# Performance work log

Measured on AMD Instinct MI355X. Metric: run time of the kernel, lower is better.

## Reference

```python
import jax, jax.numpy as jnp
import numpy as np

V, E, H, L = 32000, 256, 512, 1
B, S, T = 64, 64, 20


def setup_inputs() -> dict:
    key = jax.random.key(0)
    ks = jax.random.split(key, 12)
    return {
        "tgt_batch": jax.random.randint(ks[0], (B, T), 0, V),
        "len_src_batch": jax.random.randint(ks[1], (B,), 1, S + 1).astype(jnp.int32),
        "len_tgt_batch": jnp.full((B,), T, dtype=jnp.int32),
        "enc_final": jax.random.normal(ks[2], (L, B, H), jnp.float32),
        "enc_outputs": jax.random.normal(ks[3], (S, B, H), jnp.float32),
        "teacher_forcing": 1,
        "emb": jax.random.normal(ks[4], (V, E), jnp.float32) * 0.05,
        "W_ih": jax.random.normal(ks[5], (3 * H, E + H), jnp.float32) * 0.03,
        "W_hh": jax.random.normal(ks[6], (3 * H, H), jnp.float32) * 0.03,
        "b_ih": jnp.zeros((3 * H,), jnp.float32),
        "b_hh": jnp.zeros((3 * H,), jnp.float32),
        "W_attn": jax.random.normal(ks[7], (H, H), jnp.float32) * 0.03,
        "W_concat": jax.random.normal(ks[8], (H, 2 * H), jnp.float32) * 0.03,
        "b_concat": jnp.zeros((H,), jnp.float32),
        "W_out": jax.random.normal(ks[9], (V, H), jnp.float32) * 0.03,
        "b_out": jnp.zeros((V,), jnp.float32),
    }


def reference(tgt_batch, len_src_batch, len_tgt_batch, enc_final, enc_outputs,
              teacher_forcing, emb, W_ih, W_hh, b_ih, b_hh, W_attn,
              W_concat, b_concat, W_out, b_out):
    # source-length mask (B,S)
    src_mask = jnp.arange(S)[None, :] < len_src_batch[:, None]
    enc_bsh = enc_outputs.transpose(1, 0, 2)              # (B,S,H)
    enc_proj = jnp.einsum('bsh,gh->bsg', enc_bsh, W_attn)  # general attn: precompute W_a @ enc
    tgt_tb = tgt_batch.T                                   # (T,B)

    def gru_cell(x, h):
        gi = x @ W_ih.T + b_ih
        gh = h @ W_hh.T + b_hh
        ir, iz, inn = jnp.split(gi, 3, axis=-1)
        hr, hz, hn = jnp.split(gh, 3, axis=-1)
        r = jax.nn.sigmoid(ir + hr)
        z = jax.nn.sigmoid(iz + hz)
        n = jnp.tanh(inn + r * hn)
        return (1.0 - z) * n + z * h

    def step(carry, tok):
        h, attn_h = carry
        x = jnp.concatenate([emb[tok], attn_h], axis=-1)   # (B,E+H)
        h = gru_cell(x, h)                                 # (B,H)
        score = jnp.einsum('bh,bsh->bs', h, enc_proj)      # (B,S)
        score = jnp.where(src_mask, score, -1e9)
        aw = jax.nn.softmax(score, axis=-1)                # align weights
        ctx = jnp.einsum('bs,bsh->bh', aw, enc_bsh)        # bmm context
        attn_h = jnp.tanh(jnp.concatenate([h, ctx], -1) @ W_concat.T + b_concat)
        logits = attn_h @ W_out.T + b_out                  # (B,V)
        logp = jax.nn.log_softmax(logits, axis=-1)
        word = jnp.argmax(logp, axis=-1)
        return (h, attn_h), (logp, word)

    h0 = enc_final[0]                                      # L=1, D=1 -> (B,H)
    attn0 = jnp.zeros((B, H), jnp.float32)
    # teacher_forcing == 1: input at step t is gold token tgt[t], t = 0..T-2
    _, (dec_outputs, dec_words) = jax.lax.scan(step, (h0, attn0), tgt_tb[:-1])
    return dec_outputs, dec_words
```

## Files before the change

kernel.cpp:

```cpp
#include <hip/hip_runtime.h>
#include <math.h>

#define TSTEPS 19
#define NB 64
#define NS 64
#define NT 20
#define NH 512
#define NE 256
#define NV 32000

__device__ __forceinline__ float ldg_sys(const float* p) {
  return __hip_atomic_load(p, __ATOMIC_RELAXED, __HIP_MEMORY_SCOPE_SYSTEM);
}
__device__ __forceinline__ void stg_sys(float* p, float v) {
  __hip_atomic_store(p, v, __ATOMIC_RELAXED, __HIP_MEMORY_SCOPE_SYSTEM);
}
__device__ __forceinline__ int ldi_sys(const int* p) {
  return __hip_atomic_load(p, __ATOMIC_RELAXED, __HIP_MEMORY_SCOPE_SYSTEM);
}
__device__ __forceinline__ void sti_sys(int* p, int v) {
  __hip_atomic_store(p, v, __ATOMIC_RELAXED, __HIP_MEMORY_SCOPE_SYSTEM);
}
__device__ __forceinline__ void vmfence() {
  asm volatile("s_waitcnt vmcnt(0)" ::: "memory");
}
__device__ __forceinline__ void flag_publish(int* f) {
  vmfence();
  __syncthreads();
  if (threadIdx.x == 0) sti_sys(f, 1);
  asm volatile("" ::: "memory");
}
__device__ __forceinline__ void wait_n(const int* f, int n) {
  if (threadIdx.x < 64) {
    for (;;) {
      int ok = 1;
      for (int i = threadIdx.x; i < n; i += 64) ok &= ldi_sys(f + i);
      if (__all(ok)) break;
      __builtin_amdgcn_s_sleep(1);
    }
  }
  __syncthreads();
  asm volatile("" ::: "memory");
}

__global__ __launch_bounds__(256) void linear_kernel(
    const float* __restrict__ A, int lda,
    const float* __restrict__ W, int ldw,
    const float* __restrict__ bias,
    float* __restrict__ C, int ldc,
    int K, int act)
{
  __shared__ float As[16][68];
  __shared__ float Ws[16][132];
  const int tid = threadIdx.x;
  const int m0 = blockIdx.y * 64;
  const int n0 = blockIdx.x * 128;
  const int lr = tid >> 2;
  const int lc = (tid & 3) << 2;
  const int tm = tid & 15;
  const int tn = tid >> 4;

  float acc[4][8];
#pragma unroll
  for (int i = 0; i < 4; ++i)
#pragma unroll
    for (int j = 0; j < 8; ++j) acc[i][j] = 0.f;

  const float* Ar  = A + (size_t)(m0 + lr) * lda + lc;
  const float* Wr0 = W + (size_t)(n0 + lr) * ldw + lc;
  const float* Wr1 = W + (size_t)(n0 + 64 + lr) * ldw + lc;

  for (int kk = 0; kk < K; kk += 16) {
    float4 av = *(const float4*)(Ar + kk);
    float4 w0 = *(const float4*)(Wr0 + kk);
    float4 w1 = *(const float4*)(Wr1 + kk);
    As[lc+0][lr] = av.x; As[lc+1][lr] = av.y; As[lc+2][lr] = av.z; As[lc+3][lr] = av.w;
    Ws[lc+0][lr] = w0.x; Ws[lc+1][lr] = w0.y; Ws[lc+2][lr] = w0.z; Ws[lc+3][lr] = w0.w;
    Ws[lc+0][64+lr] = w1.x; Ws[lc+1][64+lr] = w1.y; Ws[lc+2][64+lr] = w1.z; Ws[lc+3][64+lr] = w1.w;
    __syncthreads();
#pragma unroll
    for (int k = 0; k < 16; ++k) {
      float4 a4 = *(const float4*)&As[k][tm * 4];
      float4 b4 = *(const float4*)&Ws[k][tn * 8];
      float4 b5 = *(const float4*)&Ws[k][tn * 8 + 4];
      float a[4] = {a4.x, a4.y, a4.z, a4.w};
      float b[8] = {b4.x, b4.y, b4.z, b4.w, b5.x, b5.y, b5.z, b5.w};
#pragma unroll
      for (int i = 0; i < 4; ++i)
#pragma unroll
        for (int j = 0; j < 8; ++j)
          acc[i][j] = fmaf(a[i], b[j], acc[i][j]);
    }
    __syncthreads();
  }

#pragma unroll
  for (int i = 0; i < 4; ++i) {
    int m = m0 + tm * 4 + i;
    float* crow = C + (size_t)m * ldc + n0 + tn * 8;
    float vv[8];
#pragma unroll
    for (int j = 0; j < 8; ++j) {
      float v = acc[i][j];
      if (bias) v += bias[n0 + tn * 8 + j];
      if (act == 1) v = tanhf(v);
      vv[j] = v;
    }
    *(float4*)(crow)     = make_float4(vv[0], vv[1], vv[2], vv[3]);
    *(float4*)(crow + 4) = make_float4(vv[4], vv[5], vv[6], vv[7]);
  }
}

__global__ __launch_bounds__(256) void emb_linear_kernel(
    const float* __restrict__ emb, const int* __restrict__ tgt,
    const float* __restrict__ W_ih, const float* __restrict__ b_ih,
    float* __restrict__ C)
{
  __shared__ float As[16][68];
  __shared__ float Ws[16][132];
  const int tid = threadIdx.x;
  const int m0 = blockIdx.y * 64;
  const int n0 = blockIdx.x * 128;
  const int lr = tid >> 2;
  const int lc = (tid & 3) << 2;
  const int tm = tid & 15;
  const int tn = tid >> 4;

  float acc[4][8];
#pragma unroll
  for (int i = 0; i < 4; ++i)
#pragma unroll
    for (int j = 0; j < 8; ++j) acc[i][j] = 0.f;

  const int row = m0 + lr;
  const int tok = tgt[(row & 63) * NT + (row >> 6)];
  const float* Ar  = emb + (size_t)tok * NE + lc;
  const float* Wr0 = W_ih + (size_t)(n0 + lr) * 768 + lc;
  const float* Wr1 = W_ih + (size_t)(n0 + 64 + lr) * 768 + lc;

  for (int kk = 0; kk < NE; kk += 16) {
    float4 av = *(const float4*)(Ar + kk);
    float4 w0 = *(const float4*)(Wr0 + kk);
    float4 w1 = *(const float4*)(Wr1 + kk);
    As[lc+0][lr] = av.x; As[lc+1][lr] = av.y; As[lc+2][lr] = av.z; As[lc+3][lr] = av.w;
    Ws[lc+0][lr] = w0.x; Ws[lc+1][lr] = w0.y; Ws[lc+2][lr] = w0.z; Ws[lc+3][lr] = w0.w;
    Ws[lc+0][64+lr] = w1.x; Ws[lc+1][64+lr] = w1.y; Ws[lc+2][64+lr] = w1.z; Ws[lc+3][64+lr] = w1.w;
    __syncthreads();
#pragma unroll
    for (int k = 0; k < 16; ++k) {
      float4 a4 = *(const float4*)&As[k][tm * 4];
      float4 b4 = *(const float4*)&Ws[k][tn * 8];
      float4 b5 = *(const float4*)&Ws[k][tn * 8 + 4];
      float a[4] = {a4.x, a4.y, a4.z, a4.w};
      float b[8] = {b4.x, b4.y, b4.z, b4.w, b5.x, b5.y, b5.z, b5.w};
#pragma unroll
      for (int i = 0; i < 4; ++i)
#pragma unroll
        for (int j = 0; j < 8; ++j)
          acc[i][j] = fmaf(a[i], b[j], acc[i][j]);
    }
    __syncthreads();
  }

#pragma unroll
  for (int i = 0; i < 4; ++i) {
    int m = m0 + tm * 4 + i;
    float* crow = C + (size_t)m * 1536 + n0 + tn * 8;
    float vv[8];
#pragma unroll
    for (int j = 0; j < 8; ++j) vv[j] = acc[i][j] + b_ih[n0 + tn * 8 + j];
    *(float4*)(crow)     = make_float4(vv[0], vv[1], vv[2], vv[3]);
    *(float4*)(crow + 4) = make_float4(vv[4], vv[5], vv[6], vv[7]);
  }
}

__global__ __launch_bounds__(256) void logits_kernel(
    const float* __restrict__ A, const float* __restrict__ W,
    const float* __restrict__ bias, float* __restrict__ C)
{
  const int bfl = blockIdx.x;
  const int xcd = bfl & 7;
  const int jj = bfl >> 3;
  const int mt = jj % 19;
  const int nt = xcd * 32 + jj / 19;
  if (nt >= 250) return;
  const int m0 = mt * 64;
  const int n0 = nt * 128;

  __shared__ float As[16][68];
  __shared__ float Ws[16][132];
  const int tid = threadIdx.x;
  const int lr = tid >> 2;
  const int lc = (tid & 3) << 2;
  const int tm = tid & 15;
  const int tn = tid >> 4;

  float acc[4][8];
#pragma unroll
  for (int i = 0; i < 4; ++i)
#pragma unroll
    for (int j = 0; j < 8; ++j) acc[i][j] = 0.f;

  const float* Ar  = A + (size_t)(m0 + lr) * NH + lc;
  const float* Wr0 = W + (size_t)(n0 + lr) * NH + lc;
  const float* Wr1 = W + (size_t)(n0 + 64 + lr) * NH + lc;

  for (int kk = 0; kk < NH; kk += 16) {
    float4 av = *(const float4*)(Ar + kk);
    float4 w0 = *(const float4*)(Wr0 + kk);
    float4 w1 = *(const float4*)(Wr1 + kk);
    As[lc+0][lr] = av.x; As[lc+1][lr] = av.y; As[lc+2][lr] = av.z; As[lc+3][lr] = av.w;
    Ws[lc+0][lr] = w0.x; Ws[lc+1][lr] = w0.y; Ws[lc+2][lr] = w0.z; Ws[lc+3][lr] = w0.w;
    Ws[lc+0][64+lr] = w1.x; Ws[lc+1][64+lr] = w1.y; Ws[lc+2][64+lr] = w1.z; Ws[lc+3][64+lr] = w1.w;
    __syncthreads();
#pragma unroll
    for (int k = 0; k < 16; ++k) {
      float4 a4 = *(const float4*)&As[k][tm * 4];
      float4 b4 = *(const float4*)&Ws[k][tn * 8];
      float4 b5 = *(const float4*)&Ws[k][tn * 8 + 4];
      float a[4] = {a4.x, a4.y, a4.z, a4.w};
      float b[8] = {b4.x, b4.y, b4.z, b4.w, b5.x, b5.y, b5.z, b5.w};
#pragma unroll
      for (int i = 0; i < 4; ++i)
#pragma unroll
        for (int j = 0; j < 8; ++j)
          acc[i][j] = fmaf(a[i], b[j], acc[i][j]);
    }
    __syncthreads();
  }

#pragma unroll
  for (int i = 0; i < 4; ++i) {
    int m = m0 + tm * 4 + i;
    float* crow = C + (size_t)m * NV + n0 + tn * 8;
    float vv[8];
#pragma unroll
    for (int j = 0; j < 8; ++j) vv[j] = acc[i][j] + bias[n0 + tn * 8 + j];
    *(float4*)(crow)     = make_float4(vv[0], vv[1], vv[2], vv[3]);
    *(float4*)(crow + 4) = make_float4(vv[4], vv[5], vv[6], vv[7]);
  }
}

template <int SYSA>
__device__ __forceinline__ void gemm_tile2(
    const float* __restrict__ Asrc, const float* __restrict__ W, int ldw,
    float* __restrict__ Cdst, int n0, int k0,
    float (*As)[68], float (*Ws)[68])
{
  const int tid = threadIdx.x;
  const int l = tid & 63, w = tid >> 6;
  const int m = l, nq = w;
  const int wn = tid >> 4, wc = (tid & 15) << 2;
  const int q4 = (l & 15) << 2;
  float acc[4] = {0.f, 0.f, 0.f, 0.f};
  for (int kk = 0; kk < 256; kk += 64) {
    const int kb = k0 + kk;
#pragma unroll
    for (int i = 0; i < 4; ++i) {
      const int mi = 16 * w + 4 * i + (l >> 4);
      const float* src = Asrc + (size_t)mi * NH + kb + q4;
      float4 v;
      if (SYSA) {
        v.x = ldg_sys(src); v.y = ldg_sys(src + 1);
        v.z = ldg_sys(src + 2); v.w = ldg_sys(src + 3);
      } else {
        v = *(const float4*)src;
      }
      *(float4*)&As[mi][q4] = v;
    }
    *(float4*)&Ws[wn][wc] = *(const float4*)(W + (size_t)(n0 + wn) * ldw + kb + wc);
    __syncthreads();
#pragma unroll
    for (int q = 0; q < 16; ++q) {
      float4 a4 = *(const float4*)&As[m][q * 4];
#pragma unroll
      for (int j = 0; j < 4; ++j) {
        float4 w4 = *(const float4*)&Ws[nq * 4 + j][q * 4];
        acc[j] = fmaf(a4.x, w4.x, acc[j]);
        acc[j] = fmaf(a4.y, w4.y, acc[j]);
        acc[j] = fmaf(a4.z, w4.z, acc[j]);
        acc[j] = fmaf(a4.w, w4.w, acc[j]);
      }
    }
    __syncthreads();
  }
#pragma unroll
  for (int j = 0; j < 4; ++j)
    stg_sys(Cdst + (size_t)m * 1536 + n0 + nq * 4 + j, acc[j]);
}

__global__ __launch_bounds__(256) void recur_kernel(
    const float* __restrict__ gi_emb, float* __restrict__ giA2,
    float* __restrict__ ghA2, float* __restrict__ hglob,
    float* __restrict__ attn_arr, const float* __restrict__ enc_proj,
    const float* __restrict__ enc_proj2, const float* __restrict__ enc_final,
    const int* __restrict__ len_src, const float* __restrict__ W_ih,
    const float* __restrict__ W_hh, const float* __restrict__ b_hh,
    const float* __restrict__ W_concat, const float* __restrict__ b_concat,
    int* __restrict__ flags)
{
  const int blk = blockIdx.x;
  const int tid = threadIdx.x;
  __shared__ float As[64][68];
  __shared__ float Ws[16][68];
  __shared__ float hstate[NH];
  __shared__ float scs[NS];
  __shared__ float aw[NS];

  int* ghdone = flags;
  int* gidone = flags + 4096;
  int* hdone  = flags + 8192;
  int* adone  = flags + 10240;

  if (blk >= 64) {
    const int hj = blk - 64;
    const int n0 = (hj >> 1) * 16;
    const int kh = hj & 1;
    const int k0 = kh * 256;
    float* ghD = ghA2 + kh * 98304;
    float* giD = giA2 + kh * 98304;
    gemm_tile2<0>(enc_final, W_hh, NH, ghD, n0, k0, As, Ws);
    flag_publish(ghdone + hj);
    for (int t = 0; t + 1 < TSTEPS; ++t) {
      wait_n(hdone + t * 64, 64);
      gemm_tile2<1>(hglob, W_hh, NH, ghD, n0, k0, As, Ws);
      flag_publish(ghdone + (t + 1) * 192 + hj);
      wait_n(adone + t * 64, 64);
      gemm_tile2<1>(attn_arr + (size_t)t * NB * NH, W_ih + NE, NE + NH,
                    giD, n0, k0, As, Ws);
      flag_publish(gidone + (t + 1) * 192 + hj);
    }
    return;
  }

  const int b = blk;
  hstate[tid]       = enc_final[(size_t)b * NH + tid];
  hstate[tid + 256] = enc_final[(size_t)b * NH + tid + 256];
  __syncthreads();
  const int mylen = len_src[b];

  for (int t = 0; t < TSTEPS; ++t) {
    wait_n(ghdone + t * 192, 192);
    if (t > 0) wait_n(gidone + t * 192, 192);

    const float* ge = gi_emb + (size_t)(t * NB + b) * 1536;
#pragma unroll
    for (int hh = 0; hh < 2; ++hh) {
      const int j = tid + hh * 256;
      const size_t base = (size_t)b * 1536 + j;
      float gr = ge[j];
      float gz = ge[512 + j];
      float gn = ge[1024 + j];
      if (t > 0) {
        gr += ldg_sys(giA2 + base)        + ldg_sys(giA2 + 98304 + base);
        gz += ldg_sys(giA2 + base + 512)  + ldg_sys(giA2 + 98304 + base + 512);
        gn += ldg_sys(giA2 + base + 1024) + ldg_sys(giA2 + 98304 + base + 1024);
      }
      float hr = b_hh[j]        + ldg_sys(ghA2 + base)        + ldg_sys(ghA2 + 98304 + base);
      float hz = b_hh[512 + j]  + ldg_sys(ghA2 + base + 512)  + ldg_sys(ghA2 + 98304 + base + 512);
      float hn = b_hh[1024 + j] + ldg_sys(ghA2 + base + 1024) + ldg_sys(ghA2 + 98304 + base + 1024);
      float r = 1.f / (1.f + expf(-(gr + hr)));
      float z = 1.f / (1.f + expf(-(gz + hz)));
      float n = tanhf(gn + r * hn);
      float h = (1.f - z) * n + z * hstate[j];
      hstate[j] = h;
      stg_sys(hglob + (size_t)b * NH + j, h);
    }
    vmfence();
    __syncthreads();
    if (tid == 0) sti_sys(hdone + t * 64 + b, 1);

    {
      const int s = tid >> 2, sub = tid & 3;
      const float* ep = enc_proj + ((size_t)s * NB + b) * NH + sub * 4;
      float acc = 0.f;
#pragma unroll 8
      for (int i = 0; i < 32; ++i) {
        float4 e4 = *(const float4*)(ep + i * 16);
        float4 h4 = *(const float4*)&hstate[i * 16 + sub * 4];
        acc = fmaf(e4.x, h4.x, acc); acc = fmaf(e4.y, h4.y, acc);
        acc = fmaf(e4.z, h4.z, acc); acc = fmaf(e4.w, h4.w, acc);
      }
      acc += __shfl_xor(acc, 1);
      acc += __shfl_xor(acc, 2);
      if (sub == 0) scs[s] = acc;
    }
    __syncthreads();
    if (tid < 64) {
      float v = (tid < mylen) ? scs[tid] : -1e9f;
      float mm = v;
      for (int off = 32; off >= 1; off >>= 1) mm = fmaxf(mm, __shfl_xor(mm, off));
      float e = expf(v - mm);
      float ssum = e;
      for (int off = 32; off >= 1; off >>= 1) ssum += __shfl_xor(ssum, off);
      aw[tid] = e / ssum;
    }
    __syncthreads();
    float c0 = 0.f, c1 = 0.f;
#pragma unroll 4
    for (int s2 = 0; s2 < NS; ++s2) {
      const float w = aw[s2];
      const float* e2 = enc_proj2 + ((size_t)s2 * NB + b) * NH;
      c0 = fmaf(w, e2[tid], c0);
      c1 = fmaf(w, e2[tid + 256], c1);
    }
    float* at = attn_arr + ((size_t)t * NB + b) * NH;
#pragma unroll
    for (int h2 = 0; h2 < 2; ++h2) {
      const int n = tid + h2 * 256;
      const float* wr = W_concat + (size_t)n * (2 * NH);
      float acc = 0.f;
      for (int k = 0; k < NH; k += 4) {
        float4 w4 = *(const float4*)(wr + k);
        acc = fmaf(w4.x, hstate[k],     acc);
        acc = fmaf(w4.y, hstate[k + 1], acc);
        acc = fmaf(w4.z, hstate[k + 2], acc);
        acc = fmaf(w4.w, hstate[k + 3], acc);
      }
      acc += b_concat[n] + (h2 ? c1 : c0);
      stg_sys(at + n, tanhf(acc));
    }
    vmfence();
    __syncthreads();
    if (tid == 0) sti_sys(adone + t * 64 + b, 1);
  }
}

__global__ __launch_bounds__(256) void row_softmax_kernel(
    float* __restrict__ out, float* __restrict__ words)
{
  const int row = blockIdx.x;
  const int tid = threadIdx.x;
  float* p = out + (size_t)row * NV;
  __shared__ float sm[256];
  __shared__ int   si[256];
  __shared__ float ss[256];

  float mv = -INFINITY; int mi = 0; float s = 0.f;
  for (int i = tid; i < NV; i += 256) {
    float v = p[i];
    if (v > mv) {
      s = s * expf(mv - v) + 1.f;
      mv = v; mi = i;
    } else {
      s += expf(v - mv);
    }
  }
  sm[tid] = mv; si[tid] = mi; ss[tid] = s;
  __syncthreads();
  for (int off = 128; off >= 1; off >>= 1) {
    if (tid < off) {
      float m1 = sm[tid], m2 = sm[tid + off];
      float s1 = ss[tid], s2 = ss[tid + off];
      int   i1 = si[tid], i2 = si[tid + off];
      float M = fmaxf(m1, m2);
      ss[tid] = s1 * expf(m1 - M) + s2 * expf(m2 - M);
      if (m2 > m1 || (m2 == m1 && i2 < i1)) { sm[tid] = m2; si[tid] = i2; }
    }
    __syncthreads();
  }
  const float lse = sm[0] + logf(ss[0]);
  for (int i = tid; i < NV; i += 256) p[i] -= lse;
  if (tid == 0) words[row] = (float)si[0];
}

__global__ __launch_bounds__(256) void init_kernel(int* __restrict__ flags)
{
  int i = blockIdx.x * 256 + threadIdx.x;
  if (i < 12288)
    __hip_atomic_store(flags + i, 0, __ATOMIC_RELAXED, __HIP_MEMORY_SCOPE_SYSTEM);
}

extern "C" void kernel_launch(void* const* d_in, const int* in_sizes, int n_in,
                              void* d_out, int out_size, void* d_ws, size_t ws_size,
                              hipStream_t stream) {
  const int*   tgt       = (const int*)d_in[0];
  const int*   len_src   = (const int*)d_in[1];
  const float* enc_final = (const float*)d_in[3];
  const float* enc_out   = (const float*)d_in[4];
  const float* emb       = (const float*)d_in[6];
  const float* W_ih      = (const float*)d_in[7];
  const float* W_hh      = (const float*)d_in[8];
  const float* b_ih      = (const float*)d_in[9];
  const float* b_hh      = (const float*)d_in[10];
  const float* W_attn    = (const float*)d_in[11];
  const float* W_concat  = (const float*)d_in[12];
  const float* b_concat  = (const float*)d_in[13];
  const float* W_out     = (const float*)d_in[14];
  const float* b_out     = (const float*)d_in[15];
  float* out = (float*)d_out;

  float* ws = (float*)d_ws;
  float* enc_proj = ws;
  float* gi_emb   = ws + 2097152;
  float* attn_arr = ws + 3964928;

  const size_t LOGF = (size_t)TSTEPS * NB * NV;
  float* tail = out + (LOGF - 2560000);
  float* enc_proj2 = tail;
  float* giA2  = enc_proj2 + 2097152;
  float* ghA2  = giA2 + 196608;
  float* hglob = ghA2 + 196608;
  int*   flags = (int*)(hglob + 32768);

  init_kernel<<<48, 256, 0, stream>>>(flags);

  linear_kernel<<<dim3(4, 64), 256, 0, stream>>>(
      enc_out, 512, W_attn, 512, nullptr, enc_proj, 512, 512, 0);

  linear_kernel<<<dim3(4, 64), 256, 0, stream>>>(
      enc_out, 512, W_concat + 512, 1024, nullptr, enc_proj2, 512, 512, 0);

  emb_linear_kernel<<<dim3(12, 19), 256, 0, stream>>>(
      emb, tgt, W_ih, b_ih, gi_emb);

  void* kargs[] = {
    (void*)&gi_emb, (void*)&giA2, (void*)&ghA2, (void*)&hglob,
    (void*)&attn_arr, (void*)&enc_proj, (void*)&enc_proj2, (void*)&enc_final,
    (void*)&len_src, (void*)&W_ih, (void*)&W_hh, (void*)&b_hh,
    (void*)&W_concat, (void*)&b_concat, (void*)&flags
  };
  hipLaunchCooperativeKernel((const void*)recur_kernel, dim3(256), dim3(256),
                             kargs, 0, stream);

  logits_kernel<<<4864, 256, 0, stream>>>(attn_arr, W_out, b_out, out);

  row_softmax_kernel<<<TSTEPS * NB, 256, 0, stream>>>(
      out, out + LOGF);
}
```

Baseline: 2.252 ms.

## Split recurrent GEMM helpers into separate gh and gi block groups with vectorized coherent IO

Helper blocks inside the persistent cooperative recurrence kernel now split into two groups. One group (96 blocks) computes h@W_hh and a separate group computes attn@W_ih, so the two projections run concurrently instead of serially in the same blocks. Each helper tile now covers 32 columns and a 256-wide K slice loaded in one shot, removing the inner k-loop syncs. Scalar system-scope atomics are replaced with inline-asm dwordx4 loads and stores carrying sc0 sc1 bits, and the gate math is vectorized. This raises shared memory use per block (about 100KB) and relies on hand-written cache-coherence bits for correctness.

```diff
diff --git a/kernel.cpp b/kernel.cpp
--- a/kernel.cpp
+++ b/kernel.cpp
@@ -9,12 +9,8 @@
 #define NE 256
 #define NV 32000
 
-__device__ __forceinline__ float ldg_sys(const float* p) {
-  return __hip_atomic_load(p, __ATOMIC_RELAXED, __HIP_MEMORY_SCOPE_SYSTEM);
-}
-__device__ __forceinline__ void stg_sys(float* p, float v) {
-  __hip_atomic_store(p, v, __ATOMIC_RELAXED, __HIP_MEMORY_SCOPE_SYSTEM);
-}
+typedef float f32x4 __attribute__((ext_vector_type(4)));
+
 __device__ __forceinline__ int ldi_sys(const int* p) {
   return __hip_atomic_load(p, __ATOMIC_RELAXED, __HIP_MEMORY_SCOPE_SYSTEM);
 }
@@ -23,6 +19,9 @@
 }
 __device__ __forceinline__ void vmfence() {
   asm volatile("s_waitcnt vmcnt(0)" ::: "memory");
+}
+__device__ __forceinline__ void stg4(float* p, f32x4 v) {
+  asm volatile("global_store_dwordx4 %0, %1, off sc0 sc1" :: "v"(p), "v"(v) : "memory");
 }
 __device__ __forceinline__ void flag_publish(int* f) {
   vmfence();
@@ -242,51 +241,96 @@
 }
 
 template <int SYSA>
-__device__ __forceinline__ void gemm_tile2(
+__device__ __forceinline__ void gemm_helper(
     const float* __restrict__ Asrc, const float* __restrict__ W, int ldw,
     float* __restrict__ Cdst, int n0, int k0,
-    float (*As)[68], float (*Ws)[68])
+    float (*As)[260], float (*Ws)[260])
 {
   const int tid = threadIdx.x;
-  const int l = tid & 63, w = tid >> 6;
-  const int m = l, nq = w;
-  const int wn = tid >> 4, wc = (tid & 15) << 2;
-  const int q4 = (l & 15) << 2;
-  float acc[4] = {0.f, 0.f, 0.f, 0.f};
-  for (int kk = 0; kk < 256; kk += 64) {
-    const int kb = k0 + kk;
-#pragma unroll
-    for (int i = 0; i < 4; ++i) {
-      const int mi = 16 * w + 4 * i + (l >> 4);
-      const float* src = Asrc + (size_t)mi * NH + kb + q4;
-      float4 v;
-      if (SYSA) {
-        v.x = ldg_sys(src); v.y = ldg_sys(src + 1);
-        v.z = ldg_sys(src + 2); v.w = ldg_sys(src + 3);
-      } else {
-        v = *(const float4*)src;
-      }
-      *(float4*)&As[mi][q4] = v;
-    }
-    *(float4*)&Ws[wn][wc] = *(const float4*)(W + (size_t)(n0 + wn) * ldw + kb + wc);
-    __syncthreads();
-#pragma unroll
-    for (int q = 0; q < 16; ++q) {
-      float4 a4 = *(const float4*)&As[m][q * 4];
-#pragma unroll
-      for (int j = 0; j < 4; ++j) {
-        float4 w4 = *(const float4*)&Ws[nq * 4 + j][q * 4];
-        acc[j] = fmaf(a4.x, w4.x, acc[j]);
-        acc[j] = fmaf(a4.y, w4.y, acc[j]);
-        acc[j] = fmaf(a4.z, w4.z, acc[j]);
-        acc[j] = fmaf(a4.w, w4.w, acc[j]);
-      }
-    }
-    __syncthreads();
-  }
-#pragma unroll
-  for (int j = 0; j < 4; ++j)
-    stg_sys(Cdst + (size_t)m * 1536 + n0 + nq * 4 + j, acc[j]);
+  if (SYSA) {
+    const float* s[16];
+#pragma unroll
+    for (int i = 0; i < 16; ++i) {
+      const int f = tid + (i << 8);
+      s[i] = Asrc + (size_t)(f >> 6) * NH + k0 + ((f & 63) << 2);
+    }
+    f32x4 v0,v1,v2,v3,v4,v5,v6,v7,v8,v9,v10,v11,v12,v13,v14,v15;
+    asm volatile(
+      "global_load_dwordx4 %0, %8, off sc0 sc1\n\t"
+      "global_load_dwordx4 %1, %9, off sc0 sc1\n\t"
+      "global_load_dwordx4 %2, %10, off sc0 sc1\n\t"
+      "global_load_dwordx4 %3, %11, off sc0 sc1\n\t"
+      "global_load_dwordx4 %4, %12, off sc0 sc1\n\t"
+      "global_load_dwordx4 %5, %13, off sc0 sc1\n\t"
+      "global_load_dwordx4 %6, %14, off sc0 sc1\n\t"
+      "global_load_dwordx4 %7, %15, off sc0 sc1"
+      : "=&v"(v0),"=&v"(v1),"=&v"(v2),"=&v"(v3),
+        "=&v"(v4),"=&v"(v5),"=&v"(v6),"=&v"(v7)
+      : "v"(s[0]),"v"(s[1]),"v"(s[2]),"v"(s[3]),
+        "v"(s[4]),"v"(s[5]),"v"(s[6]),"v"(s[7])
+      : "memory");
+    asm volatile(
+      "global_load_dwordx4 %0, %8, off sc0 sc1\n\t"
+      "global_load_dwordx4 %1, %9, off sc0 sc1\n\t"
+      "global_load_dwordx4 %2, %10, off sc0 sc1\n\t"
+      "global_load_dwordx4 %3, %11, off sc0 sc1\n\t"
+      "global_load_dwordx4 %4, %12, off sc0 sc1\n\t"
+      "global_load_dwordx4 %5, %13, off sc0 sc1\n\t"
+      "global_load_dwordx4 %6, %14, off sc0 sc1\n\t"
+      "global_load_dwordx4 %7, %15, off sc0 sc1\n\t"
+      "s_waitcnt vmcnt(0)"
+      : "=&v"(v8),"=&v"(v9),"=&v"(v10),"=&v"(v11),
+        "=&v"(v12),"=&v"(v13),"=&v"(v14),"=&v"(v15)
+      : "v"(s[8]),"v"(s[9]),"v"(s[10]),"v"(s[11]),
+        "v"(s[12]),"v"(s[13]),"v"(s[14]),"v"(s[15])
+      : "memory");
+    __builtin_amdgcn_sched_barrier(0);
+    f32x4 vv[16] = {v0,v1,v2,v3,v4,v5,v6,v7,v8,v9,v10,v11,v12,v13,v14,v15};
+#pragma unroll
+    for (int i = 0; i < 16; ++i) {
+      const int f = tid + (i << 8);
+      *(f32x4*)&As[f >> 6][(f & 63) << 2] = vv[i];
+    }
+  } else {
+#pragma unroll
+    for (int i = 0; i < 16; ++i) {
+      const int f = tid + (i << 8);
+      *(f32x4*)&As[f >> 6][(f & 63) << 2] =
+          *(const f32x4*)(Asrc + (size_t)(f >> 6) * NH + k0 + ((f & 63) << 2));
+    }
+  }
+#pragma unroll
+  for (int i = 0; i < 8; ++i) {
+    const int f = tid + (i << 8);
+    *(f32x4*)&Ws[f >> 6][(f & 63) << 2] =
+        *(const f32x4*)(W + (size_t)(n0 + (f >> 6)) * ldw + k0 + ((f & 63) << 2));
+  }
+  __syncthreads();
+  const int tm = tid & 31, tn = tid >> 5;
+  float acc[2][4] = {{0.f,0.f,0.f,0.f},{0.f,0.f,0.f,0.f}};
+#pragma unroll 2
+  for (int q = 0; q < 64; ++q) {
+    f32x4 a0 = *(const f32x4*)&As[tm][q << 2];
+    f32x4 a1 = *(const f32x4*)&As[tm + 32][q << 2];
+#pragma unroll
+    for (int jj = 0; jj < 4; ++jj) {
+      f32x4 w4 = *(const f32x4*)&Ws[(tn << 2) + jj][q << 2];
+      float t0 = acc[0][jj];
+      t0 = fmaf(a0.x, w4.x, t0); t0 = fmaf(a0.y, w4.y, t0);
+      t0 = fmaf(a0.z, w4.z, t0); t0 = fmaf(a0.w, w4.w, t0);
+      acc[0][jj] = t0;
+      float t1 = acc[1][jj];
+      t1 = fmaf(a1.x, w4.x, t1); t1 = fmaf(a1.y, w4.y, t1);
+      t1 = fmaf(a1.z, w4.z, t1); t1 = fmaf(a1.w, w4.w, t1);
+      acc[1][jj] = t1;
+    }
+  }
+  __syncthreads();
+  f32x4 r0 = {acc[0][0], acc[0][1], acc[0][2], acc[0][3]};
+  f32x4 r1 = {acc[1][0], acc[1][1], acc[1][2], acc[1][3]};
+  float* p0 = Cdst + (size_t)tm * 1536 + n0 + (tn << 2);
+  stg4(p0, r0);
+  stg4(p0 + 32 * 1536, r1);
 }
 
 __global__ __launch_bounds__(256) void recur_kernel(
@@ -301,34 +345,35 @@
 {
   const int blk = blockIdx.x;
   const int tid = threadIdx.x;
-  __shared__ float As[64][68];
-  __shared__ float Ws[16][68];
+  __shared__ float As[64][260];
+  __shared__ float Ws[32][260];
   __shared__ float hstate[NH];
+  __shared__ float uext[NH];
   __shared__ float scs[NS];
   __shared__ float aw[NS];
 
-  int* ghdone = flags;
-  int* gidone = flags + 4096;
-  int* hdone  = flags + 8192;
-  int* adone  = flags + 10240;
-
+  if (blk >= 160) {
+    const int hj = blk - 160;
+    const int n0 = (hj >> 1) * 32, kh = hj & 1, k0 = kh * 256;
+    float* giD = giA2 + kh * 98304;
+    for (int t = 0; t + 1 < TSTEPS; ++t) {
+      wait_n(flags + 6400 + t * 64, 64);
+      gemm_helper<1>(attn_arr + (size_t)t * NB * NH, W_ih + NE, NE + NH,
+                     giD, n0, k0, As, Ws);
+      flag_publish(flags + (t + 1) * 256 + 96 + hj);
+    }
+    return;
+  }
   if (blk >= 64) {
     const int hj = blk - 64;
-    const int n0 = (hj >> 1) * 16;
-    const int kh = hj & 1;
-    const int k0 = kh * 256;
+    const int n0 = (hj >> 1) * 32, kh = hj & 1, k0 = kh * 256;
     float* ghD = ghA2 + kh * 98304;
-    float* giD = giA2 + kh * 98304;
-    gemm_tile2<0>(enc_final, W_hh, NH, ghD, n0, k0, As, Ws);
-    flag_publish(ghdone + hj);
+    gemm_helper<0>(enc_final, W_hh, NH, ghD, n0, k0, As, Ws);
+    flag_publish(flags + hj);
     for (int t = 0; t + 1 < TSTEPS; ++t) {
-      wait_n(hdone + t * 64, 64);
-      gemm_tile2<1>(hglob, W_hh, NH, ghD, n0, k0, As, Ws);
-      flag_publish(ghdone + (t + 1) * 192 + hj);
-      wait_n(adone + t * 64, 64);
-      gemm_tile2<1>(attn_arr + (size_t)t * NB * NH, W_ih + NE, NE + NH,
-                    giD, n0, k0, As, Ws);
-      flag_publish(gidone + (t + 1) * 192 + hj);
+      wait_n(flags + 5120 + t * 64, 64);
+      gemm_helper<1>(hglob, W_hh, NH, ghD, n0, k0, As, Ws);
+      flag_publish(flags + (t + 1) * 256 + hj);
     }
     return;
   }
@@ -340,35 +385,86 @@
   const int mylen = len_src[b];
 
   for (int t = 0; t < TSTEPS; ++t) {
-    wait_n(ghdone + t * 192, 192);
-    if (t > 0) wait_n(gidone + t * 192, 192);
-
-    const float* ge = gi_emb + (size_t)(t * NB + b) * 1536;
-#pragma unroll
-    for (int hh = 0; hh < 2; ++hh) {
-      const int j = tid + hh * 256;
+    if (t == 0) wait_n(flags, 96);
+    else        wait_n(flags + t * 256, 192);
+
+    if (tid < 128) {
+      const int j = tid << 2;
+      const float* ge = gi_emb + (size_t)(t * NB + b) * 1536;
+      f32x4 er = *(const f32x4*)(ge + j);
+      f32x4 ez = *(const f32x4*)(ge + 512 + j);
+      f32x4 en = *(const f32x4*)(ge + 1024 + j);
+      f32x4 br = *(const f32x4*)(b_hh + j);
+      f32x4 bz = *(const f32x4*)(b_hh + 512 + j);
+      f32x4 bn = *(const f32x4*)(b_hh + 1024 + j);
       const size_t base = (size_t)b * 1536 + j;
-      float gr = ge[j];
-      float gz = ge[512 + j];
-      float gn = ge[1024 + j];
+      f32x4 I0,I1,I2,I3,I4,I5, G0,G1,G2,G3,G4,G5;
       if (t > 0) {
-        gr += ldg_sys(giA2 + base)        + ldg_sys(giA2 + 98304 + base);
-        gz += ldg_sys(giA2 + base + 512)  + ldg_sys(giA2 + 98304 + base + 512);
-        gn += ldg_sys(giA2 + base + 1024) + ldg_sys(giA2 + 98304 + base + 1024);
+        const float* q0 = giA2 + base;          const float* q1 = q0 + 512;
+        const float* q2 = q0 + 1024;
+        const float* q3 = giA2 + 98304 + base;  const float* q4 = q3 + 512;
+        const float* q5 = q3 + 1024;
+        const float* r0 = ghA2 + base;          const float* r1 = r0 + 512;
+        const float* r2 = r0 + 1024;
+        const float* r3 = ghA2 + 98304 + base;  const float* r4 = r3 + 512;
+        const float* r5 = r3 + 1024;
+        asm volatile(
+          "global_load_dwordx4 %0, %12, off sc0 sc1\n\t"
+          "global_load_dwordx4 %1, %13, off sc0 sc1\n\t"
+          "global_load_dwordx4 %2, %14, off sc0 sc1\n\t"
+          "global_load_dwordx4 %3, %15, off sc0 sc1\n\t"
+          "global_load_dwordx4 %4, %16, off sc0 sc1\n\t"
+          "global_load_dwordx4 %5, %17, off sc0 sc1\n\t"
+          "global_load_dwordx4 %6, %18, off sc0 sc1\n\t"
+          "global_load_dwordx4 %7, %19, off sc0 sc1\n\t"
+          "global_load_dwordx4 %8, %20, off sc0 sc1\n\t"
+          "global_load_dwordx4 %9, %21, off sc0 sc1\n\t"
+          "global_load_dwordx4 %10, %22, off sc0 sc1\n\t"
+          "global_load_dwordx4 %11, %23, off sc0 sc1\n\t"
+          "s_waitcnt vmcnt(0)"
+          : "=&v"(I0),"=&v"(I1),"=&v"(I2),"=&v"(I3),"=&v"(I4),"=&v"(I5),
+            "=&v"(G0),"=&v"(G1),"=&v"(G2),"=&v"(G3),"=&v"(G4),"=&v"(G5)
+          : "v"(q0),"v"(q1),"v"(q2),"v"(q3),"v"(q4),"v"(q5),
+            "v"(r0),"v"(r1),"v"(r2),"v"(r3),"v"(r4),"v"(r5)
+          : "memory");
+      } else {
+        const float* r0 = ghA2 + base;          const float* r1 = r0 + 512;
+        const float* r2 = r0 + 1024;
+        const float* r3 = ghA2 + 98304 + base;  const float* r4 = r3 + 512;
+        const float* r5 = r3 + 1024;
+        asm volatile(
+          "global_load_dwordx4 %0, %6, off sc0 sc1\n\t"
+          "global_load_dwordx4 %1, %7, off sc0 sc1\n\t"
+          "global_load_dwordx4 %2, %8, off sc0 sc1\n\t"
+          "global_load_dwordx4 %3, %9, off sc0 sc1\n\t"
+          "global_load_dwordx4 %4, %10, off sc0 sc1\n\t"
+          "global_load_dwordx4 %5, %11, off sc0 sc1\n\t"
+          "s_waitcnt vmcnt(0)"
+          : "=&v"(G0),"=&v"(G1),"=&v"(G2),"=&v"(G3),"=&v"(G4),"=&v"(G5)
+          : "v"(r0),"v"(r1),"v"(r2),"v"(r3),"v"(r4),"v"(r5)
+          : "memory");
+        I0 = I1 = I2 = I3 = I4 = I5 = (f32x4){0.f, 0.f, 0.f, 0.f};
       }
-      float hr = b_hh[j]        + ldg_sys(ghA2 + base)        + ldg_sys(ghA2 + 98304 + base);
-      float hz = b_hh[512 + j]  + ldg_sys(ghA2 + base + 512)  + ldg_sys(ghA2 + 98304 + base + 512);
-      float hn = b_hh[1024 + j] + ldg_sys(ghA2 + base + 1024) + ldg_sys(ghA2 + 98304 + base + 1024);
-      float r = 1.f / (1.f + expf(-(gr + hr)));
-      float z = 1.f / (1.f + expf(-(gz + hz)));
-      float n = tanhf(gn + r * hn);
-      float h = (1.f - z) * n + z * hstate[j];
-      hstate[j] = h;
-      stg_sys(hglob + (size_t)b * NH + j, h);
-    }
-    vmfence();
-    __syncthreads();
-    if (tid == 0) sti_sys(hdone + t * 64 + b, 1);
+      __builtin_amdgcn_sched_barrier(0);
+      f32x4 GR = I0 + I3 + er;
+      f32x4 GZ = I1 + I4 + ez;
+      f32x4 GN = I2 + I5 + en;
+      f32x4 HR = G0 + G3 + br;
+      f32x4 HZ = G1 + G4 + bz;
+      f32x4 HN = G2 + G5 + bn;
+      f32x4 hold = *(f32x4*)&hstate[j];
+      f32x4 hv;
+#define GATEC(c) { \
+      float r_ = 1.f / (1.f + expf(-(GR.c + HR.c))); \
+      float z_ = 1.f / (1.f + expf(-(GZ.c + HZ.c))); \
+      float n_ = tanhf(GN.c + r_ * HN.c); \
+      hv.c = (1.f - z_) * n_ + z_ * hold.c; }
+      GATEC(x) GATEC(y) GATEC(z) GATEC(w)
+#undef GATEC
+      *(f32x4*)&hstate[j] = hv;
+      stg4(hglob + (size_t)b * NH + j, hv);
+    }
+    flag_publish(flags + 5120 + t * 64 + b);
 
     {
       const int s = tid >> 2, sub = tid & 3;
@@ -376,8 +472,8 @@
       float acc = 0.f;
 #pragma unroll 8
       for (int i = 0; i < 32; ++i) {
-        float4 e4 = *(const float4*)(ep + i * 16);
-        float4 h4 = *(const float4*)&hstate[i * 16 + sub * 4];
+        f32x4 e4 = *(const f32x4*)(ep + i * 16);
+        f32x4 h4 = *(const f32x4*)&hstate[i * 16 + sub * 4];
         acc = fmaf(e4.x, h4.x, acc); acc = fmaf(e4.y, h4.y, acc);
         acc = fmaf(e4.z, h4.z, acc); acc = fmaf(e4.w, h4.w, acc);
       }
@@ -404,25 +500,28 @@
       c0 = fmaf(w, e2[tid], c0);
       c1 = fmaf(w, e2[tid + 256], c1);
     }
-    float* at = attn_arr + ((size_t)t * NB + b) * NH;
 #pragma unroll
     for (int h2 = 0; h2 < 2; ++h2) {
       const int n = tid + h2 * 256;
       const float* wr = W_concat + (size_t)n * (2 * NH);
       float acc = 0.f;
       for (int k = 0; k < NH; k += 4) {
-        float4 w4 = *(const float4*)(wr + k);
+        f32x4 w4 = *(const f32x4*)(wr + k);
         acc = fmaf(w4.x, hstate[k],     acc);
         acc = fmaf(w4.y, hstate[k + 1], acc);
         acc = fmaf(w4.z, hstate[k + 2], acc);
         acc = fmaf(w4.w, hstate[k + 3], acc);
       }
-      acc += b_concat[n] + (h2 ? c1 : c0);
-      stg_sys(at + n, tanhf(acc));
-    }
-    vmfence();
-    __syncthreads();
-    if (tid == 0) sti_sys(adone + t * 64 + b, 1);
+      uext[n] = acc + b_concat[n] + (h2 ? c1 : c0);
+    }
+    __syncthreads();
+    if (tid < 128) {
+      const int j = tid << 2;
+      f32x4 u4 = *(f32x4*)&uext[j];
+      f32x4 a4 = {tanhf(u4.x), tanhf(u4.y), tanhf(u4.z), tanhf(u4.w)};
+      stg4(attn_arr + ((size_t)t * NB + b) * NH + j, a4);
+    }
+    flag_publish(flags + 6400 + t * 64 + b);
   }
 }
 
@@ -467,7 +566,7 @@
 __global__ __launch_bounds__(256) void init_kernel(int* __restrict__ flags)
 {
   int i = blockIdx.x * 256 + threadIdx.x;
-  if (i < 12288)
+  if (i < 8192)
     __hip_atomic_store(flags + i, 0, __ATOMIC_RELAXED, __HIP_MEMORY_SCOPE_SYSTEM);
 }
 
@@ -503,7 +602,7 @@
   float* hglob = ghA2 + 196608;
   int*   flags = (int*)(hglob + 32768);
 
-  init_kernel<<<48, 256, 0, stream>>>(flags);
+  init_kernel<<<32, 256, 0, stream>>>(flags);
 
   linear_kernel<<<dim3(4, 64), 256, 0, stream>>>(
       enc_out, 512, W_attn, 512, nullptr, enc_proj, 512, 512, 0);
@@ -525,6 +624,5 @@
 
   logits_kernel<<<4864, 256, 0, stream>>>(attn_arr, W_out, b_out, out);
 
-  row_softmax_kernel<<<TSTEPS * NB, 256, 0, stream>>>(
-      out, out + LOGF);
-}
+  row_softmax_kernel<<<TSTEPS * NB, 256, 0, stream>>>(out, out + LOGF);
+}
```

Result: faster. 2.003 ms (-11.1%).

## Split recurrent GEMMs across dedicated block groups with per-step buffers

Applied to the files above, without the earlier changes.

The persistent recurrent kernel now uses 512-thread blocks. The hidden-state GEMM and the attention-input GEMM move to separate block groups (96 blocks each), so they run concurrently instead of back to back in the same blocks. Per-timestep buffers for h, gi and gh replace the single reused buffers, which removes write-after-read hazards. System-scope scalar atomic loads are replaced by plain vector loads, and stores become dwordx4 with sc0 sc1 bits. Each GEMM tile now stages the full 256-wide K slice in LDS at once, giving larger LDS use. The risk is that plain loads of data written by other blocks could be stale without system-scope semantics.

```diff
diff --git a/kernel.cpp b/kernel.cpp
--- a/kernel.cpp
+++ b/kernel.cpp
@@ -9,12 +9,8 @@
 #define NE 256
 #define NV 32000
 
-__device__ __forceinline__ float ldg_sys(const float* p) {
-  return __hip_atomic_load(p, __ATOMIC_RELAXED, __HIP_MEMORY_SCOPE_SYSTEM);
-}
-__device__ __forceinline__ void stg_sys(float* p, float v) {
-  __hip_atomic_store(p, v, __ATOMIC_RELAXED, __HIP_MEMORY_SCOPE_SYSTEM);
-}
+typedef float f32x4 __attribute__((ext_vector_type(4)));
+
 __device__ __forceinline__ int ldi_sys(const int* p) {
   return __hip_atomic_load(p, __ATOMIC_RELAXED, __HIP_MEMORY_SCOPE_SYSTEM);
 }
@@ -23,6 +19,9 @@
 }
 __device__ __forceinline__ void vmfence() {
   asm volatile("s_waitcnt vmcnt(0)" ::: "memory");
+}
+__device__ __forceinline__ void stg4(float* p, f32x4 v) {
+  asm volatile("global_store_dwordx4 %0, %1, off sc0 sc1" :: "v"(p), "v"(v) : "memory");
 }
 __device__ __forceinline__ void flag_publish(int* f) {
   vmfence();
@@ -241,57 +240,47 @@
   }
 }
 
-template <int SYSA>
-__device__ __forceinline__ void gemm_tile2(
+__device__ __forceinline__ void gemm_helper(
     const float* __restrict__ Asrc, const float* __restrict__ W, int ldw,
     float* __restrict__ Cdst, int n0, int k0,
-    float (*As)[68], float (*Ws)[68])
+    float (*As)[260], float (*Ws)[260])
 {
   const int tid = threadIdx.x;
-  const int l = tid & 63, w = tid >> 6;
-  const int m = l, nq = w;
-  const int wn = tid >> 4, wc = (tid & 15) << 2;
-  const int q4 = (l & 15) << 2;
+#pragma unroll
+  for (int i = 0; i < 8; ++i) {
+    const int f = tid + (i << 9);
+    const int r = f >> 6, c = (f & 63) << 2;
+    *(f32x4*)&As[r][c] = *(const f32x4*)(Asrc + (size_t)r * NH + k0 + c);
+  }
+#pragma unroll
+  for (int i = 0; i < 4; ++i) {
+    const int f = tid + (i << 9);
+    const int r = f >> 6, c = (f & 63) << 2;
+    *(f32x4*)&Ws[r][c] = *(const f32x4*)(W + (size_t)(n0 + r) * ldw + k0 + c);
+  }
+  __syncthreads();
+  const int tm = tid & 63, tn = tid >> 6;
   float acc[4] = {0.f, 0.f, 0.f, 0.f};
-  for (int kk = 0; kk < 256; kk += 64) {
-    const int kb = k0 + kk;
-#pragma unroll
-    for (int i = 0; i < 4; ++i) {
-      const int mi = 16 * w + 4 * i + (l >> 4);
-      const float* src = Asrc + (size_t)mi * NH + kb + q4;
-      float4 v;
-      if (SYSA) {
-        v.x = ldg_sys(src); v.y = ldg_sys(src + 1);
-        v.z = ldg_sys(src + 2); v.w = ldg_sys(src + 3);
-      } else {
-        v = *(const float4*)src;
-      }
-      *(float4*)&As[mi][q4] = v;
-    }
-    *(float4*)&Ws[wn][wc] = *(const float4*)(W + (size_t)(n0 + wn) * ldw + kb + wc);
-    __syncthreads();
-#pragma unroll
-    for (int q = 0; q < 16; ++q) {
-      float4 a4 = *(const float4*)&As[m][q * 4];
-#pragma unroll
-      for (int j = 0; j < 4; ++j) {
-        float4 w4 = *(const float4*)&Ws[nq * 4 + j][q * 4];
-        acc[j] = fmaf(a4.x, w4.x, acc[j]);
-        acc[j] = fmaf(a4.y, w4.y, acc[j]);
-        acc[j] = fmaf(a4.z, w4.z, acc[j]);
-        acc[j] = fmaf(a4.w, w4.w, acc[j]);
-      }
-    }
-    __syncthreads();
-  }
-#pragma unroll
-  for (int j = 0; j < 4; ++j)
-    stg_sys(Cdst + (size_t)m * 1536 + n0 + nq * 4 + j, acc[j]);
-}
-
-__global__ __launch_bounds__(256) void recur_kernel(
-    const float* __restrict__ gi_emb, float* __restrict__ giA2,
-    float* __restrict__ ghA2, float* __restrict__ hglob,
+#pragma unroll 4
+  for (int q = 0; q < 64; ++q) {
+    f32x4 a4 = *(const f32x4*)&As[tm][q << 2];
+#pragma unroll
+    for (int j = 0; j < 4; ++j) {
+      f32x4 w4 = *(const f32x4*)&Ws[(tn << 2) + j][q << 2];
+      float t0 = acc[j];
+      t0 = fmaf(a4.x, w4.x, t0); t0 = fmaf(a4.y, w4.y, t0);
+      t0 = fmaf(a4.z, w4.z, t0); t0 = fmaf(a4.w, w4.w, t0);
+      acc[j] = t0;
+    }
+  }
+  __syncthreads();
+  f32x4 r = {acc[0], acc[1], acc[2], acc[3]};
+  stg4(Cdst + (size_t)tm * 1536 + n0 + (tn << 2), r);
+}
+
+__global__ __launch_bounds__(512) void recur_kernel(
+    const float* __restrict__ gi_emb, float* __restrict__ giP,
+    float* __restrict__ ghP, float* __restrict__ hbuf,
     float* __restrict__ attn_arr, const float* __restrict__ enc_proj,
     const float* __restrict__ enc_proj2, const float* __restrict__ enc_final,
     const int* __restrict__ len_src, const float* __restrict__ W_ih,
@@ -301,88 +290,104 @@
 {
   const int blk = blockIdx.x;
   const int tid = threadIdx.x;
-  __shared__ float As[64][68];
-  __shared__ float Ws[16][68];
+  __shared__ float As[64][260];
+  __shared__ float Ws[32][260];
   __shared__ float hstate[NH];
+  __shared__ float uext[NH];
   __shared__ float scs[NS];
   __shared__ float aw[NS];
 
-  int* ghdone = flags;
-  int* gidone = flags + 4096;
-  int* hdone  = flags + 8192;
-  int* adone  = flags + 10240;
-
+  int* hdone = flags + 3648;
+  int* adone = flags + 4864;
+
+  if (blk >= 160) {
+    const int hj = blk - 160;
+    const int n0 = (hj >> 1) * 32, kh = hj & 1, k0 = kh * 256;
+    for (int t = 0; t + 1 < TSTEPS; ++t) {
+      wait_n(adone + t * 64, 64);
+      gemm_helper(attn_arr + (size_t)t * NB * NH, W_ih + NE, NE + NH,
+                  giP + (size_t)(t + 1) * 196608 + kh * 98304, n0, k0, As, Ws);
+      flag_publish(flags + (t + 1) * 192 + 96 + hj);
+    }
+    return;
+  }
   if (blk >= 64) {
     const int hj = blk - 64;
-    const int n0 = (hj >> 1) * 16;
-    const int kh = hj & 1;
-    const int k0 = kh * 256;
-    float* ghD = ghA2 + kh * 98304;
-    float* giD = giA2 + kh * 98304;
-    gemm_tile2<0>(enc_final, W_hh, NH, ghD, n0, k0, As, Ws);
-    flag_publish(ghdone + hj);
+    const int n0 = (hj >> 1) * 32, kh = hj & 1, k0 = kh * 256;
+    gemm_helper(enc_final, W_hh, NH, ghP + kh * 98304, n0, k0, As, Ws);
+    flag_publish(flags + hj);
     for (int t = 0; t + 1 < TSTEPS; ++t) {
       wait_n(hdone + t * 64, 64);
-      gemm_tile2<1>(hglob, W_hh, NH, ghD, n0, k0, As, Ws);
-      flag_publish(ghdone + (t + 1) * 192 + hj);
-      wait_n(adone + t * 64, 64);
-      gemm_tile2<1>(attn_arr + (size_t)t * NB * NH, W_ih + NE, NE + NH,
-                    giD, n0, k0, As, Ws);
-      flag_publish(gidone + (t + 1) * 192 + hj);
+      gemm_helper(hbuf + (size_t)t * NB * NH, W_hh, NH,
+                  ghP + (size_t)(t + 1) * 196608 + kh * 98304, n0, k0, As, Ws);
+      flag_publish(flags + (t + 1) * 192 + hj);
     }
     return;
   }
 
   const int b = blk;
-  hstate[tid]       = enc_final[(size_t)b * NH + tid];
-  hstate[tid + 256] = enc_final[(size_t)b * NH + tid + 256];
+  if (tid < 256) {
+    hstate[tid]       = enc_final[(size_t)b * NH + tid];
+    hstate[tid + 256] = enc_final[(size_t)b * NH + tid + 256];
+  }
   __syncthreads();
   const int mylen = len_src[b];
 
   for (int t = 0; t < TSTEPS; ++t) {
-    wait_n(ghdone + t * 192, 192);
-    if (t > 0) wait_n(gidone + t * 192, 192);
-
-    const float* ge = gi_emb + (size_t)(t * NB + b) * 1536;
-#pragma unroll
-    for (int hh = 0; hh < 2; ++hh) {
-      const int j = tid + hh * 256;
+    wait_n(flags + t * 192, t == 0 ? 96 : 192);
+
+    if (tid < 128) {
+      const int j = tid << 2;
+      const float* ge = gi_emb + (size_t)(t * NB + b) * 1536;
+      f32x4 GR = *(const f32x4*)(ge + j);
+      f32x4 GZ = *(const f32x4*)(ge + 512 + j);
+      f32x4 GN = *(const f32x4*)(ge + 1024 + j);
       const size_t base = (size_t)b * 1536 + j;
-      float gr = ge[j];
-      float gz = ge[512 + j];
-      float gn = ge[1024 + j];
-      if (t > 0) {
-        gr += ldg_sys(giA2 + base)        + ldg_sys(giA2 + 98304 + base);
-        gz += ldg_sys(giA2 + base + 512)  + ldg_sys(giA2 + 98304 + base + 512);
-        gn += ldg_sys(giA2 + base + 1024) + ldg_sys(giA2 + 98304 + base + 1024);
+      {
+        const float* g0 = ghP + (size_t)t * 196608 + base;
+        const float* g1 = g0 + 98304;
+        f32x4 HR = *(const f32x4*)(b_hh + j)        + *(const f32x4*)(g0)
+                 + *(const f32x4*)(g1);
+        f32x4 HZ = *(const f32x4*)(b_hh + 512 + j)  + *(const f32x4*)(g0 + 512)
+                 + *(const f32x4*)(g1 + 512);
+        f32x4 HN = *(const f32x4*)(b_hh + 1024 + j) + *(const f32x4*)(g0 + 1024)
+                 + *(const f32x4*)(g1 + 1024);
+        if (t > 0) {
+          const float* q0 = giP + (size_t)t * 196608 + base;
+          const float* q1 = q0 + 98304;
+          GR += *(const f32x4*)(q0)        + *(const f32x4*)(q1);
+          GZ += *(const f32x4*)(q0 + 512)  + *(const f32x4*)(q1 + 512);
+          GN += *(const f32x4*)(q0 + 1024) + *(const f32x4*)(q1 + 1024);
+        }
+        f32x4 hold = *(f32x4*)&hstate[j];
+        f32x4 hv;
+#define GATEC(c) { \
+        float r_ = 1.f / (1.f + expf(-(GR.c + HR.c))); \
+        float z_ = 1.f / (1.f + expf(-(GZ.c + HZ.c))); \
+        float n_ = tanhf(GN.c + r_ * HN.c); \
+        hv.c = (1.f - z_) * n_ + z_ * hold.c; }
+        GATEC(x) GATEC(y) GATEC(z) GATEC(w)
+#undef GATEC
+        *(f32x4*)&hstate[j] = hv;
+        stg4(hbuf + (size_t)t * NB * NH + (size_t)b * NH + j, hv);
       }
-      float hr = b_hh[j]        + ldg_sys(ghA2 + base)        + ldg_sys(ghA2 + 98304 + base);
-      float hz = b_hh[512 + j]  + ldg_sys(ghA2 + base + 512)  + ldg_sys(ghA2 + 98304 + base + 512);
-      float hn = b_hh[1024 + j] + ldg_sys(ghA2 + base + 1024) + ldg_sys(ghA2 + 98304 + base + 1024);
-      float r = 1.f / (1.f + expf(-(gr + hr)));
-      float z = 1.f / (1.f + expf(-(gz + hz)));
-      float n = tanhf(gn + r * hn);
-      float h = (1.f - z) * n + z * hstate[j];
-      hstate[j] = h;
-      stg_sys(hglob + (size_t)b * NH + j, h);
-    }
-    vmfence();
-    __syncthreads();
-    if (tid == 0) sti_sys(hdone + t * 64 + b, 1);
+    }
+    flag_publish(hdone + t * 64 + b);
 
     {
-      const int s = tid >> 2, sub = tid & 3;
+      const int s = tid >> 3, sub = tid & 7;
       const float* ep = enc_proj + ((size_t)s * NB + b) * NH + sub * 4;
       float acc = 0.f;
-#pragma unroll 8
-      for (int i = 0; i < 32; ++i) {
-        float4 e4 = *(const float4*)(ep + i * 16);
-        float4 h4 = *(const float4*)&hstate[i * 16 + sub * 4];
+#pragma unroll
+      for (int i = 0; i < 16; ++i) {
+        f32x4 e4 = *(const f32x4*)(ep + i * 32);
+        f32x4 h4 = *(const f32x4*)&hstate[i * 32 + sub * 4];
         acc = fmaf(e4.x, h4.x, acc); acc = fmaf(e4.y, h4.y, acc);
         acc = fmaf(e4.z, h4.z, acc); acc = fmaf(e4.w, h4.w, acc);
       }
       acc += __shfl_xor(acc, 1);
       acc += __shfl_xor(acc, 2);
+      acc += __shfl_xor(acc, 4);
       if (sub == 0) scs[s] = acc;
     }
     __syncthreads();
@@ -396,33 +401,31 @@
       aw[tid] = e / ssum;
     }
     __syncthreads();
-    float c0 = 0.f, c1 = 0.f;
+    {
+      const int n = tid;
+      float c = 0.f;
 #pragma unroll 4
-    for (int s2 = 0; s2 < NS; ++s2) {
-      const float w = aw[s2];
-      const float* e2 = enc_proj2 + ((size_t)s2 * NB + b) * NH;
-      c0 = fmaf(w, e2[tid], c0);
-      c1 = fmaf(w, e2[tid + 256], c1);
-    }
-    float* at = attn_arr + ((size_t)t * NB + b) * NH;
-#pragma unroll
-    for (int h2 = 0; h2 < 2; ++h2) {
-      const int n = tid + h2 * 256;
+      for (int s2 = 0; s2 < NS; ++s2)
+        c = fmaf(aw[s2], enc_proj2[(size_t)s2 * NB * NH + (size_t)b * NH + n], c);
       const float* wr = W_concat + (size_t)n * (2 * NH);
       float acc = 0.f;
       for (int k = 0; k < NH; k += 4) {
-        float4 w4 = *(const float4*)(wr + k);
+        f32x4 w4 = *(const f32x4*)(wr + k);
         acc = fmaf(w4.x, hstate[k],     acc);
         acc = fmaf(w4.y, hstate[k + 1], acc);
         acc = fmaf(w4.z, hstate[k + 2], acc);
         acc = fmaf(w4.w, hstate[k + 3], acc);
       }
-      acc += b_concat[n] + (h2 ? c1 : c0);
-      stg_sys(at + n, tanhf(acc));
-    }
-    vmfence();
-    __syncthreads();
-    if (tid == 0) sti_sys(adone + t * 64 + b, 1);
+      uext[n] = acc + b_concat[n] + c;
+    }
+    __syncthreads();
+    if (tid < 128) {
+      const int j = tid << 2;
+      f32x4 u4 = *(f32x4*)&uext[j];
+      f32x4 a4 = {tanhf(u4.x), tanhf(u4.y), tanhf(u4.z), tanhf(u4.w)};
+      stg4(attn_arr + ((size_t)t * NB + b) * NH + j, a4);
+    }
+    flag_publish(adone + t * 64 + b);
   }
 }
 
@@ -467,7 +470,7 @@
 __global__ __launch_bounds__(256) void init_kernel(int* __restrict__ flags)
 {
   int i = blockIdx.x * 256 + threadIdx.x;
-  if (i < 12288)
+  if (i < 8192)
     __hip_atomic_store(flags + i, 0, __ATOMIC_RELAXED, __HIP_MEMORY_SCOPE_SYSTEM);
 }
 
@@ -496,14 +499,15 @@
   float* attn_arr = ws + 3964928;
 
   const size_t LOGF = (size_t)TSTEPS * NB * NV;
-  float* tail = out + (LOGF - 2560000);
+  const size_t SCRATCH = 2097152 + 3735552 + 3735552 + 622592 + 8192;
+  float* tail = out + (LOGF - SCRATCH);
   float* enc_proj2 = tail;
-  float* giA2  = enc_proj2 + 2097152;
-  float* ghA2  = giA2 + 196608;
-  float* hglob = ghA2 + 196608;
-  int*   flags = (int*)(hglob + 32768);
-
-  init_kernel<<<48, 256, 0, stream>>>(flags);
+  float* ghP  = enc_proj2 + 2097152;
+  float* giP  = ghP + 3735552;
+  float* hbuf = giP + 3735552;
+  int*   flags = (int*)(hbuf + 622592);
+
+  init_kernel<<<32, 256, 0, stream>>>(flags);
 
   linear_kernel<<<dim3(4, 64), 256, 0, stream>>>(
       enc_out, 512, W_attn, 512, nullptr, enc_proj, 512, 512, 0);
@@ -515,16 +519,15 @@
       emb, tgt, W_ih, b_ih, gi_emb);
 
   void* kargs[] = {
-    (void*)&gi_emb, (void*)&giA2, (void*)&ghA2, (void*)&hglob,
+    (void*)&gi_emb, (void*)&giP, (void*)&ghP, (void*)&hbuf,
     (void*)&attn_arr, (void*)&enc_proj, (void*)&enc_proj2, (void*)&enc_final,
     (void*)&len_src, (void*)&W_ih, (void*)&W_hh, (void*)&b_hh,
     (void*)&W_concat, (void*)&b_concat, (void*)&flags
   };
-  hipLaunchCooperativeKernel((const void*)recur_kernel, dim3(256), dim3(256),
+  hipLaunchCooperativeKernel((const void*)recur_kernel, dim3(256), dim3(512),
                              kargs, 0, stream);
 
   logits_kernel<<<4864, 256, 0, stream>>>(attn_arr, W_out, b_out, out);
 
-  row_softmax_kernel<<<TSTEPS * NB, 256, 0, stream>>>(
-      out, out + LOGF);
-}
+  row_softmax_kernel<<<TSTEPS * NB, 256, 0, stream>>>(out, out + LOGF);
+}
```

New measurement: 1.964 ms. -12.8%, faster.
